# Kernel tuning notes

Hardware: AMD Instinct MI355X
Metric: run time of the kernel (lower is better)

Reference implementation:

```python
import jax, jax.numpy as jnp
import numpy as np
from jax import lax

K = 4
OUT_PLANES = 128
TEMPERATURE = 30.0


def setup_inputs() -> dict:
    key = jax.random.key(0)
    ks = jax.random.split(key, 5)
    in_planes, k = 128, 3
    he_std = float(np.sqrt(2.0)) * (in_planes * k * k) ** (-0.5)
    return {
        "x": jax.random.normal(ks[0], (16, in_planes, 64, 64), jnp.float32),
        "weight": jax.random.normal(ks[1], (K * OUT_PLANES, in_planes, k, k), jnp.float32) * he_std,
        "bias": jax.random.normal(ks[2], (K * OUT_PLANES,), jnp.float32) * 0.01,
        "se_w1": jax.random.normal(ks[3], (33, in_planes), jnp.float32) * (2.0 / 33) ** 0.5,
        "se_w2": jax.random.normal(ks[4], (K, 33), jnp.float32) * (2.0 / K) ** 0.5,
        "se_b2": jnp.zeros((K,), jnp.float32),
    }


def reference(x, weight, bias, se_w1, se_w2, se_b2):
    B = x.shape[0]
    # SE attention: global avg pool -> fc1 -> relu -> fc2 -> softmax(./T)
    pooled = x.mean(axis=(2, 3))                      # [B, Cin]
    h = jax.nn.relu(pooled @ se_w1.T)                 # [B, hidden]
    logits = h @ se_w2.T + se_b2                      # [B, K]
    attn = jax.nn.softmax(logits / TEMPERATURE, axis=1)
    # conv with K*out channels (groups=1, stride=1, pad=1, dil=1)
    y = lax.conv_general_dilated(
        x, weight, window_strides=(1, 1), padding=[(1, 1), (1, 1)],
        dimension_numbers=("NCHW", "OIHW", "NCHW"))
    y = y + bias[None, :, None, None]                 # [B, K*out, Ho, Wo]
    Ho, Wo = y.shape[2], y.shape[3]
    y = y.reshape(B, K, OUT_PLANES, Ho, Wo)
    # attention-weighted combine over K branches (bmm in torch)
    return jnp.einsum("bk,bkohw->bohw", attn, y)
```

## Files before the change

### kernel.cpp

```cpp
#include <hip/hip_runtime.h>
#include <cstdint>
#include <cstddef>

typedef unsigned short u16;
typedef __attribute__((ext_vector_type(8))) short short8;
typedef __attribute__((ext_vector_type(4))) float f32x4;

__device__ __forceinline__ u16 f2bf(float f){
  union { float f; unsigned u; } c; c.f = f;
  unsigned u = c.u;
  u += 0x7fffu + ((u >> 16) & 1u);
  return (u16)(u >> 16);
}
__device__ __forceinline__ unsigned pk2(float a, float b){
  union { float f; unsigned u; } ca, cb; ca.f = a; cb.f = b;
  return ((ca.u + 0x8000u) >> 16) | ((cb.u + 0x8000u) & 0xFFFF0000u);
}

#define XB_STRIDE 557568
#define XR_STRIDE 8448

#define GLD_LDS(gsrc, ldst) \
  __builtin_amdgcn_global_load_lds((const __attribute__((address_space(1))) void*)(gsrc), \
                                   (__attribute__((address_space(3))) void*)(ldst), 16, 0, 0)

__global__ __launch_bounds__(256) void xpose_pool(
    const float* __restrict__ x, u16* __restrict__ xT2, float* __restrict__ part)
{
  const int bid = blockIdx.x;
  const int b = bid & 15, chunk = bid >> 4;
  const int pos0 = chunk << 7;
  const int tid = threadIdx.x;
  __shared__ u16 tile[16384];
  __shared__ float psum[128 * 33];
  const float* xb = x + ((size_t)b << 19) + pos0;
  const int p4 = (tid & 31) << 2;
  const int swz = (tid & 31) & 7;

  if (chunk == 0){
    u16* xh = xT2 + (size_t)b * XB_STRIDE;
    for (int i = tid; i < 4160; i += 256){
      const int p = i >> 4, oct = i & 15;
      int row, col;
      if (p < 66)      { row = 0;        col = p; }
      else if (p < 132){ row = 65;       col = p - 66; }
      else if (p < 196){ row = p - 131;  col = 0; }
      else             { row = p - 195;  col = 65; }
      *(uint4*)(xh + row * XR_STRIDE + (col << 7) + (oct << 3)) =
          make_uint4(0u, 0u, 0u, 0u);
    }
  }

  #pragma unroll
  for (int i = 0; i < 2; ++i){
    const int gci = (tid >> 5) + (i << 3);
    const int ci8 = gci << 3;
    float4 L[8];
    #pragma unroll
    for (int j = 0; j < 8; ++j)
      L[j] = *(const float4*)(xb + ((size_t)(ci8 + j) << 12) + p4);
    #pragma unroll
    for (int j = 0; j < 8; ++j)
      psum[(ci8 + j) * 33 + (tid & 31)] = L[j].x + L[j].y + L[j].z + L[j].w;
    const int gs = gci ^ swz;
    const float* e = (const float*)L;
    #pragma unroll
    for (int p = 0; p < 4; ++p){
      const int row = p4 + p;
      uint4 V;
      V.x = pk2(e[0 * 4 + p], e[1 * 4 + p]);
      V.y = pk2(e[2 * 4 + p], e[3 * 4 + p]);
      V.z = pk2(e[4 * 4 + p], e[5 * 4 + p]);
      V.w = pk2(e[6 * 4 + p], e[7 * 4 + p]);
      *(uint4*)(tile + (row << 7) + (gs << 3)) = V;
    }
  }
  __syncthreads();

  if (tid < 128){
    float s = 0.f;
    #pragma unroll 8
    for (int j = 0; j < 32; ++j) s += psum[tid * 33 + j];
    part[((b << 5) + chunk) * 128 + tid] = s;
  }

  u16* xo = xT2 + (size_t)b * XB_STRIDE;
  const int g = tid & 15, rb = (tid >> 4) << 3;
  #pragma unroll
  for (int r = 0; r < 8; ++r){
    const int row = rb + r;
    const int gs = g ^ ((row >> 2) & 7);
    uint4 v = *(const uint4*)(tile + (row << 7) + (gs << 3));
    const int pos = pos0 + row;
    const int h = pos >> 6, w = pos & 63;
    *(uint4*)(xo + (h + 1) * XR_STRIDE + ((w + 1) << 7) + (g << 3)) = v;
  }
}

__global__ void attn_fc(const float* __restrict__ part, const float* __restrict__ w1,
                        const float* __restrict__ w2, const float* __restrict__ b2,
                        float* __restrict__ attn)
{
  const int b = blockIdx.x, t = threadIdx.x;
  __shared__ float sp[128];
  __shared__ float sh[33];
  __shared__ float sl[4];
  const float* pb = part + (b << 12);
  float s = 0.f;
  for (int c = 0; c < 32; ++c) s += pb[(c << 7) + t];
  sp[t] = s * (1.f / 4096.f);
  __syncthreads();
  if (t < 33){
    float h = 0.f;
    for (int ci = 0; ci < 128; ++ci) h += sp[ci] * w1[t * 128 + ci];
    sh[t] = fmaxf(h, 0.f);
  }
  __syncthreads();
  if (t < 4){
    float l = b2[t];
    for (int j = 0; j < 33; ++j) l += sh[j] * w2[t * 33 + j];
    sl[t] = l * (1.f / 30.f);
  }
  __syncthreads();
  if (t == 0){
    float m = fmaxf(fmaxf(sl[0], sl[1]), fmaxf(sl[2], sl[3]));
    float e0 = __expf(sl[0] - m), e1 = __expf(sl[1] - m);
    float e2 = __expf(sl[2] - m), e3 = __expf(sl[3] - m);
    float inv = 1.f / (e0 + e1 + e2 + e3);
    attn[(b << 2) + 0] = e0 * inv; attn[(b << 2) + 1] = e1 * inv;
    attn[(b << 2) + 2] = e2 * inv; attn[(b << 2) + 3] = e3 * inv;
  }
}

__global__ __launch_bounds__(256) void combine(
    const float* __restrict__ W, const float* __restrict__ bias,
    const float* __restrict__ attn, u16* __restrict__ wcomb,
    float* __restrict__ bcomb)
{
  const int bid = blockIdx.x;
  const int b = bid & 15, q = bid >> 4;
  const int tid = threadIdx.x;
  const float a0 = attn[(b << 2) + 0], a1 = attn[(b << 2) + 1];
  const float a2 = attn[(b << 2) + 2], a3 = attn[(b << 2) + 3];
  if (tid < 2){
    const int co = (q << 1) + tid;
    bcomb[(b << 7) + co] = a0 * bias[co] + a1 * bias[128 + co]
                         + a2 * bias[256 + co] + a3 * bias[384 + co];
  }
  u16* wob = wcomb + (size_t)b * 147456;
  for (int gi = tid; gi < 288; gi += 256){
    const int co_l = gi / 144;
    const int r = gi - co_l * 144;
    const int tap = r >> 4;
    const int gg = r & 15;
    const int c = gg >> 3, g = gg & 7;
    const int co = (q << 1) + co_l;
    union { u16 h[8]; uint4 v; } pk;
    #pragma unroll
    for (int e = 0; e < 8; ++e){
      const int ci = (c << 6) + (g << 3) + e;
      const size_t woff = (size_t)(co << 7 | ci) * 9 + tap;
      float s = a0 * W[woff]          + a1 * W[147456 + woff]
              + a2 * W[294912 + woff] + a3 * W[442368 + woff];
      pk.h[e] = f2bf(s);
    }
    *(uint4*)(wob + (size_t)(tap * 2 + c) * 8192 + (co << 6) + ((g ^ (co & 7)) << 3)) = pk.v;
  }
}

__global__ __launch_bounds__(256, 2) void conv_mfma(
    const u16* __restrict__ xT2, const u16* __restrict__ wcomb,
    const float* __restrict__ bcomb, float* __restrict__ out)
{
  extern __shared__ char smem[];
  u16* s_x = (u16*)smem;
  u16* s_w = (u16*)(smem + 33792);

  const int tid = threadIdx.x;
  const int lane = tid & 63, wid = tid >> 6;
  const int wr = wid & 1, wcv = wid >> 1;
  const int l15 = lane & 15, hi = lane >> 4;
  const int sw7 = l15 & 7;

  const int bid = blockIdx.x;
  const int b = bid & 15;
  const int h0 = (bid >> 4) << 1;

  const u16* Abase = wcomb + (size_t)b * 147456;
  const u16* Xbase = xT2 + (size_t)b * XB_STRIDE;

#define STAGE_X(C) { \
    _Pragma("unroll") \
    for (int _it = 0; _it < 9; ++_it){ \
      const int _G = _it * 256 + tid; \
      if (_it < 8 || _G < 2112){ \
        const int _oct = _G & 7, _t = _G >> 3; \
        const int _col = _t % 66, _row = _t / 66; \
        const u16* _src = Xbase + (h0 + _row) * XR_STRIDE + (_col << 7) \
                        + ((C) << 6) + ((_oct ^ (_col & 7)) << 3); \
        GLD_LDS(_src, s_x + (_G << 3)); \
      } \
    } }

#define STAGE_W(SLAB, BUF) { \
    const u16* _As = Abase + (size_t)(SLAB) * 8192; \
    u16* _sw = s_w + (BUF) * 8192; \
    _Pragma("unroll") \
    for (int _it = 0; _it < 4; ++_it){ \
      const int _G = _it * 256 + tid; \
      GLD_LDS(_As + (_G << 3), _sw + (_G << 3)); \
    } }

#define COMPUTE(S, BUF) { \
    const int _tap = (S) < 9 ? (S) : (S) - 9; \
    const int _dh = _tap / 3, _dw = _tap - 3 * _dh; \
    const int _b7 = (l15 + _dw) & 7; \
    const u16* _sw = s_w + (BUF) * 8192; \
    _Pragma("unroll") \
    for (int _ks = 0; _ks < 2; ++_ks){ \
      const int _k4 = (_ks << 2) + hi; \
      short8 _af[4], _bf[4]; \
      _Pragma("unroll") \
      for (int _a = 0; _a < 4; ++_a){ \
        const int _co = (wcv << 6) + (_a << 4) + l15; \
        _af[_a] = *(const short8*)(_sw + (_co << 6) + ((_k4 ^ sw7) << 3)); \
      } \
      _Pragma("unroll") \
      for (int _p = 0; _p < 4; ++_p){ \
        const int _col = l15 + _dw + (_p << 4); \
        _bf[_p] = *(const short8*)(s_x + ((((wr + _dh) * 66 + _col) << 3) \
                                          + (_k4 ^ _b7)) * 8); \
      } \
      _Pragma("unroll") \
      for (int _a = 0; _a < 4; ++_a) \
        _Pragma("unroll") \
        for (int _p = 0; _p < 4; ++_p) \
          acc[_a][_p] = __builtin_amdgcn_mfma_f32_16x16x32_bf16(_af[_a], _bf[_p], acc[_a][_p], 0, 0, 0); \
    } }

#define VM0_BAR { asm volatile("s_waitcnt vmcnt(0)" ::: "memory"); __syncthreads(); }

  f32x4 acc[4][4] = {};

  STAGE_X(0);
  STAGE_W(0, 0);
  VM0_BAR;

  for (int s = 0; s < 8; ++s){
    STAGE_W(2 * (s + 1), (s & 1) ^ 1);
    COMPUTE(s, s & 1);
    VM0_BAR;
  }
  STAGE_W(1, 1);
  COMPUTE(8, 0);
  VM0_BAR;
  STAGE_X(1);
  VM0_BAR;
  for (int s = 9; s < 17; ++s){
    STAGE_W(2 * (s + 1 - 9) + 1, (s & 1) ^ 1);
    COMPUTE(s, s & 1);
    VM0_BAR;
  }
  COMPUTE(17, 1);

#undef VM0_BAR
#undef COMPUTE
#undef STAGE_W
#undef STAGE_X

  const int hrow = h0 + wr;
  float* ob = out + ((size_t)b << 19) + (hrow << 6) + l15;
  #pragma unroll
  for (int a = 0; a < 4; ++a){
    const int co0 = (wcv << 6) + (a << 4) + (hi << 2);
    #pragma unroll
    for (int r = 0; r < 4; ++r){
      const float bc = bcomb[(b << 7) + co0 + r];
      float* op = ob + (size_t)(co0 + r) * 4096;
      #pragma unroll
      for (int p = 0; p < 4; ++p)
        __builtin_nontemporal_store(acc[a][p][r] + bc, op + (p << 4));
    }
  }
}

extern "C" void kernel_launch(void* const* d_in, const int* in_sizes, int n_in,
                              void* d_out, int out_size, void* d_ws, size_t ws_size,
                              hipStream_t stream)
{
  const float* x    = (const float*)d_in[0];
  const float* W    = (const float*)d_in[1];
  const float* bias = (const float*)d_in[2];
  const float* w1   = (const float*)d_in[3];
  const float* w2   = (const float*)d_in[4];
  const float* b2   = (const float*)d_in[5];
  float* out = (float*)d_out;

  char* ws = (char*)d_ws;
  float* part  = (float*)(ws);
  float* attn  = (float*)(ws + 262144);
  float* bcomb = (float*)(ws + 262400);
  u16*   xT2   = (u16*)  (ws + 270592);
  u16*   wcomb = (u16*)  (ws + 18112768);

  xpose_pool<<<512, 256, 0, stream>>>(x, xT2, part);
  attn_fc<<<16, 128, 0, stream>>>(part, w1, w2, b2, attn);
  combine<<<1024, 256, 0, stream>>>(W, bias, attn, wcomb, bcomb);

  (void)hipFuncSetAttribute(reinterpret_cast<const void*>(conv_mfma),
                            hipFuncAttributeMaxDynamicSharedMemorySize, 66560);
  conv_mfma<<<512, 256, 66560, stream>>>(xT2, wcomb, bcomb, out);
}
```

Baseline: 56.37 us.

## Halve conv K-chunk to 32 channels to cut LDS, stage combine weights in LDS

The conv kernel now processes input channels in four 32-channel chunks instead of two 64-channel chunks. This halves the shared memory for the x tile and weight buffers (about 33 KB instead of 66 KB) so more blocks can be resident per CU. It also drops the XOR swizzle, and the weight layout in the combine kernel is changed to match. The combine kernel now stages its weight rows into LDS with coalesced global-to-LDS loads instead of strided scalar global reads. The trade-off is twice as many pipeline steps and barriers with less MFMA work per step, and possible LDS bank conflicts now that the swizzle is gone.

Result: faster. 50.06 us (-11.2%).

```diff
diff --git a/kernel.cpp b/kernel.cpp
--- a/kernel.cpp
+++ b/kernel.cpp
@@ -19,6 +19,7 @@
 
 #define XB_STRIDE 557568
 #define XR_STRIDE 8448
+
 
 #define GLD_LDS(gsrc, ldst) \
   __builtin_amdgcn_global_load_lds((const __attribute__((address_space(1))) void*)(gsrc), \
@@ -137,34 +138,48 @@
     const float* __restrict__ attn, u16* __restrict__ wcomb,
     float* __restrict__ bcomb)
 {
+  __shared__ float wlds[9216];
   const int bid = blockIdx.x;
-  const int b = bid & 15, q = bid >> 4;
+  const int b = bid & 15, cp = bid >> 4;
   const int tid = threadIdx.x;
   const float a0 = attn[(b << 2) + 0], a1 = attn[(b << 2) + 1];
   const float a2 = attn[(b << 2) + 2], a3 = attn[(b << 2) + 3];
+
+  #pragma unroll
+  for (int it = 0; it < 9; ++it){
+    const int G = it * 256 + tid;
+    const int k = G / 576, rem = G - k * 576;
+    const int co_l = rem / 288, j4 = rem - co_l * 288;
+    const float* src = W + (size_t)(k * 128 + (cp << 1) + co_l) * 1152 + (j4 << 2);
+    GLD_LDS(src, (char*)wlds + (G << 4));
+  }
+
   if (tid < 2){
-    const int co = (q << 1) + tid;
+    const int co = (cp << 1) + tid;
     bcomb[(b << 7) + co] = a0 * bias[co] + a1 * bias[128 + co]
                          + a2 * bias[256 + co] + a3 * bias[384 + co];
   }
+  asm volatile("s_waitcnt vmcnt(0)" ::: "memory");
+  __syncthreads();
+
   u16* wob = wcomb + (size_t)b * 147456;
   for (int gi = tid; gi < 288; gi += 256){
     const int co_l = gi / 144;
     const int r = gi - co_l * 144;
     const int tap = r >> 4;
     const int gg = r & 15;
-    const int c = gg >> 3, g = gg & 7;
-    const int co = (q << 1) + co_l;
+    const int cq = gg >> 2, g = gg & 3;
+    const int co = (cp << 1) + co_l;
     union { u16 h[8]; uint4 v; } pk;
     #pragma unroll
     for (int e = 0; e < 8; ++e){
-      const int ci = (c << 6) + (g << 3) + e;
-      const size_t woff = (size_t)(co << 7 | ci) * 9 + tap;
-      float s = a0 * W[woff]          + a1 * W[147456 + woff]
-              + a2 * W[294912 + woff] + a3 * W[442368 + woff];
+      const int ci = (cq << 5) + (g << 3) + e;
+      const int j = ci * 9 + tap;
+      float s = a0 * wlds[co_l * 1152 + j]        + a1 * wlds[2304 + co_l * 1152 + j]
+              + a2 * wlds[4608 + co_l * 1152 + j] + a3 * wlds[6912 + co_l * 1152 + j];
       pk.h[e] = f2bf(s);
     }
-    *(uint4*)(wob + (size_t)(tap * 2 + c) * 8192 + (co << 6) + ((g ^ (co & 7)) << 3)) = pk.v;
+    *(uint4*)(wob + (((tap << 2) + cq) << 12) + (co << 5) + (g << 3)) = pk.v;
   }
 }
 
@@ -174,13 +189,12 @@
 {
   extern __shared__ char smem[];
   u16* s_x = (u16*)smem;
-  u16* s_w = (u16*)(smem + 33792);
+  u16* s_w = (u16*)(smem + 16896);
 
   const int tid = threadIdx.x;
   const int lane = tid & 63, wid = tid >> 6;
   const int wr = wid & 1, wcv = wid >> 1;
   const int l15 = lane & 15, hi = lane >> 4;
-  const int sw7 = l15 & 7;
 
   const int bid = blockIdx.x;
   const int b = bid & 15;
@@ -189,79 +203,71 @@
   const u16* Abase = wcomb + (size_t)b * 147456;
   const u16* Xbase = xT2 + (size_t)b * XB_STRIDE;
 
-#define STAGE_X(C) { \
+#define STAGE_X(Q) { \
     _Pragma("unroll") \
-    for (int _it = 0; _it < 9; ++_it){ \
+    for (int _it = 0; _it < 5; ++_it){ \
       const int _G = _it * 256 + tid; \
-      if (_it < 8 || _G < 2112){ \
-        const int _oct = _G & 7, _t = _G >> 3; \
+      if (_it < 4 || _G < 1056){ \
+        const int _oct = _G & 3, _t = _G >> 2; \
         const int _col = _t % 66, _row = _t / 66; \
         const u16* _src = Xbase + (h0 + _row) * XR_STRIDE + (_col << 7) \
-                        + ((C) << 6) + ((_oct ^ (_col & 7)) << 3); \
+                        + ((Q) << 5) + (_oct << 3); \
         GLD_LDS(_src, s_x + (_G << 3)); \
       } \
     } }
 
-#define STAGE_W(SLAB, BUF) { \
-    const u16* _As = Abase + (size_t)(SLAB) * 8192; \
-    u16* _sw = s_w + (BUF) * 8192; \
+#define STAGE_W(Q, TAP, BUF) { \
+    const u16* _As = Abase + (((((TAP) << 2) + (Q))) << 12); \
+    u16* _sw = s_w + (BUF) * 4096; \
+    GLD_LDS(_As + (tid << 3), _sw + (tid << 3)); \
+    GLD_LDS(_As + ((tid + 256) << 3), _sw + ((tid + 256) << 3)); }
+
+#define COMPUTE(TAP, BUF) { \
+    const int _dh = (TAP) / 3, _dw = (TAP) - 3 * (_dh); \
+    const u16* _sw = s_w + (BUF) * 4096; \
+    short8 _af[4], _bf[4]; \
     _Pragma("unroll") \
-    for (int _it = 0; _it < 4; ++_it){ \
-      const int _G = _it * 256 + tid; \
-      GLD_LDS(_As + (_G << 3), _sw + (_G << 3)); \
-    } }
-
-#define COMPUTE(S, BUF) { \
-    const int _tap = (S) < 9 ? (S) : (S) - 9; \
-    const int _dh = _tap / 3, _dw = _tap - 3 * _dh; \
-    const int _b7 = (l15 + _dw) & 7; \
-    const u16* _sw = s_w + (BUF) * 8192; \
+    for (int _a = 0; _a < 4; ++_a){ \
+      const int _co = (wcv << 6) + (_a << 4) + l15; \
+      _af[_a] = *(const short8*)(_sw + (_co << 5) + (hi << 3)); \
+    } \
     _Pragma("unroll") \
-    for (int _ks = 0; _ks < 2; ++_ks){ \
-      const int _k4 = (_ks << 2) + hi; \
-      short8 _af[4], _bf[4]; \
+    for (int _p = 0; _p < 4; ++_p){ \
+      const int _col = l15 + _dw + (_p << 4); \
+      _bf[_p] = *(const short8*)(s_x + (((wr + _dh) * 66 + _col) << 5) + (hi << 3)); \
+    } \
+    _Pragma("unroll") \
+    for (int _a = 0; _a < 4; ++_a) \
       _Pragma("unroll") \
-      for (int _a = 0; _a < 4; ++_a){ \
-        const int _co = (wcv << 6) + (_a << 4) + l15; \
-        _af[_a] = *(const short8*)(_sw + (_co << 6) + ((_k4 ^ sw7) << 3)); \
-      } \
-      _Pragma("unroll") \
-      for (int _p = 0; _p < 4; ++_p){ \
-        const int _col = l15 + _dw + (_p << 4); \
-        _bf[_p] = *(const short8*)(s_x + ((((wr + _dh) * 66 + _col) << 3) \
-                                          + (_k4 ^ _b7)) * 8); \
-      } \
-      _Pragma("unroll") \
-      for (int _a = 0; _a < 4; ++_a) \
-        _Pragma("unroll") \
-        for (int _p = 0; _p < 4; ++_p) \
-          acc[_a][_p] = __builtin_amdgcn_mfma_f32_16x16x32_bf16(_af[_a], _bf[_p], acc[_a][_p], 0, 0, 0); \
-    } }
+      for (int _p = 0; _p < 4; ++_p) \
+        acc[_a][_p] = __builtin_amdgcn_mfma_f32_16x16x32_bf16(_af[_a], _bf[_p], acc[_a][_p], 0, 0, 0); }
 
 #define VM0_BAR { asm volatile("s_waitcnt vmcnt(0)" ::: "memory"); __syncthreads(); }
 
   f32x4 acc[4][4] = {};
 
   STAGE_X(0);
-  STAGE_W(0, 0);
+  STAGE_W(0, 0, 0);
   VM0_BAR;
 
-  for (int s = 0; s < 8; ++s){
-    STAGE_W(2 * (s + 1), (s & 1) ^ 1);
-    COMPUTE(s, s & 1);
-    VM0_BAR;
-  }
-  STAGE_W(1, 1);
-  COMPUTE(8, 0);
-  VM0_BAR;
-  STAGE_X(1);
-  VM0_BAR;
-  for (int s = 9; s < 17; ++s){
-    STAGE_W(2 * (s + 1 - 9) + 1, (s & 1) ^ 1);
-    COMPUTE(s, s & 1);
-    VM0_BAR;
-  }
-  COMPUTE(17, 1);
+  int buf = 0;
+  for (int q = 0; q < 4; ++q){
+    #pragma unroll
+    for (int tap = 0; tap < 9; ++tap){
+      if (!(q == 3 && tap == 8)){
+        const int nq = (tap == 8) ? q + 1 : q;
+        const int nt = (tap == 8) ? 0 : tap + 1;
+        STAGE_W(nq, nt, buf ^ 1);
+      }
+      COMPUTE(tap, buf);
+      VM0_BAR;
+      buf ^= 1;
+      if (tap == 8 && q < 3){
+        STAGE_X(q + 1);
+        VM0_BAR;
+      }
+    }
+  }
 
 #undef VM0_BAR
 #undef COMPUTE
@@ -308,6 +314,6 @@
   combine<<<1024, 256, 0, stream>>>(W, bias, attn, wcomb, bcomb);
 
   (void)hipFuncSetAttribute(reinterpret_cast<const void*>(conv_mfma),
-                            hipFuncAttributeMaxDynamicSharedMemorySize, 66560);
-  conv_mfma<<<512, 256, 66560, stream>>>(xT2, wcomb, bcomb, out);
-}
+                            hipFuncAttributeMaxDynamicSharedMemorySize, 33280);
+  conv_mfma<<<512, 256, 33280, stream>>>(xT2, wcomb, bcomb, out);
+}
```
